# Kernel optimization log

Measured on AMD Instinct MI355X. Metric: run time of the kernel, lower is better.

The kernel has to match this reference:

```python
import jax, jax.numpy as jnp
import numpy as np

NUM_LAYERS = 4
B, L, D = 8, 512, 512
H, F = 8, 2048
HD = D // H
EPS = 1e-5


def _layernorm(x, g, b):
    mu = jnp.mean(x, axis=-1, keepdims=True)
    var = jnp.var(x, axis=-1, keepdims=True)
    return (x - mu) * jax.lax.rsqrt(var + EPS) * g + b


def setup_inputs() -> dict:
    key = jax.random.key(0)
    ks = jax.random.split(key, 14)
    s = 0.02
    return {
        "src": jax.random.normal(ks[0], (B, L, D), dtype=jnp.float32),
        "Wqkv": jax.random.normal(ks[1], (NUM_LAYERS, 3 * D, D), dtype=jnp.float32) * s,
        "bqkv": jnp.zeros((NUM_LAYERS, 3 * D), dtype=jnp.float32),
        "Wo": jax.random.normal(ks[2], (NUM_LAYERS, D, D), dtype=jnp.float32) * s,
        "bo": jnp.zeros((NUM_LAYERS, D), dtype=jnp.float32),
        "W1": jax.random.normal(ks[3], (NUM_LAYERS, F, D), dtype=jnp.float32) * s,
        "b1": jnp.zeros((NUM_LAYERS, F), dtype=jnp.float32),
        "W2": jax.random.normal(ks[4], (NUM_LAYERS, D, F), dtype=jnp.float32) * s,
        "b2": jnp.zeros((NUM_LAYERS, D), dtype=jnp.float32),
        "g1": jnp.ones((NUM_LAYERS, D), dtype=jnp.float32),
        "be1": jnp.zeros((NUM_LAYERS, D), dtype=jnp.float32),
        "g2": jnp.ones((NUM_LAYERS, D), dtype=jnp.float32),
        "be2": jnp.zeros((NUM_LAYERS, D), dtype=jnp.float32),
    }


def reference(src, Wqkv, bqkv, Wo, bo, W1, b1, W2, b2, g1, be1, g2, be2):
    x = src
    attns = []
    scale = 1.0 / np.sqrt(HD).astype(np.float32)
    for i in range(NUM_LAYERS):
        # --- self attention (need_weights=True, average_attn_weights=False) ---
        qkv = x @ Wqkv[i].T + bqkv[i]                      # [B,L,3D]
        q, k, v = jnp.split(qkv, 3, axis=-1)
        q = q.reshape(B, L, H, HD).transpose(0, 2, 1, 3)   # [B,H,L,hd]
        k = k.reshape(B, L, H, HD).transpose(0, 2, 1, 3)
        v = v.reshape(B, L, H, HD).transpose(0, 2, 1, 3)
        scores = jnp.einsum("bhld,bhsd->bhls", q * scale, k)
        attn = jax.nn.softmax(scores, axis=-1)             # [B,H,L,S]
        attns.append(attn)
        ctx = jnp.einsum("bhls,bhsd->bhld", attn, v)
        ctx = ctx.transpose(0, 2, 1, 3).reshape(B, L, D)
        attn_out = ctx @ Wo[i].T + bo[i]
        # --- post-norm residual + FFN ---
        x = _layernorm(x + attn_out, g1[i], be1[i])
        ff = jax.nn.relu(x @ W1[i].T + b1[i]) @ W2[i].T + b2[i]
        x = _layernorm(x + ff, g2[i], be2[i])
    return x, jnp.stack(attns)  # ([B,L,D], [num_layers,B,H,L,S])
```

## Files before the change

kernel.cpp:

```cpp
#include <hip/hip_runtime.h>
#include <hip/hip_bf16.h>

#define B_ 8
#define L_ 512
#define D_ 512
#define H_ 8
#define F_ 2048
#define NL_ 4
#define BL 4096
#define EPS_ 1e-5f

typedef __bf16 bf16_t;
typedef bf16_t bf16x8 __attribute__((ext_vector_type(8)));
typedef float f32x4 __attribute__((ext_vector_type(4)));
typedef unsigned short u16x4 __attribute__((ext_vector_type(4)));

__device__ __forceinline__ unsigned short f2b_rn(float f) {
  unsigned u = __builtin_bit_cast(unsigned, f);
  u = (u + 0x7fffu + ((u >> 16) & 1u)) >> 16;
  return (unsigned short)u;
}

__device__ __forceinline__ void gload_lds16(const unsigned short* g, unsigned short* l) {
  __builtin_amdgcn_global_load_lds(
      (const __attribute__((address_space(1))) void*)g,
      (__attribute__((address_space(3))) void*)l, 16, 0, 0);
}

template<int BM, int BN, int MT, int NT>
__global__ __launch_bounds__(256)
void gemm_bt(const unsigned short* __restrict__ A, int lda, long sAo, long sAi,
             const unsigned short* __restrict__ Bm, int ldb, long sBo, long sBi,
             float* __restrict__ Cf, unsigned short* __restrict__ Cb, int ldc,
             long sCo, long sCi,
             const float* __restrict__ bias, int K, float scale, int relu, int zi)
{
  static_assert(BM == MT * 32 && BN == NT * 32, "waves are 2x2");
  __shared__ unsigned short As[BM * 32];
  __shared__ unsigned short Bs[BN * 32];
  const int tid  = threadIdx.x;
  const int lane = tid & 63;
  const int wave = tid >> 6;
  const int wm = (wave >> 1) * (MT * 16);
  const int wn = (wave & 1) * (NT * 16);
  const int m0 = blockIdx.x * BM;
  const int n0 = blockIdx.y * BN;
  const int z  = blockIdx.z;
  const long offA = (long)(z / zi) * sAo + (long)(z % zi) * sAi;
  const long offB = (long)(z / zi) * sBo + (long)(z % zi) * sBi;
  const long offC = (long)(z / zi) * sCo + (long)(z % zi) * sCi;

  f32x4 acc[MT][NT] = {};

  for (int k0 = 0; k0 < K; k0 += 32) {
    __syncthreads();
#pragma unroll
    for (int j = 0; j < BM / 64; ++j) {
      int c = tid + j * 256;
      int r = c >> 2, cc = (c & 3) * 8;
      gload_lds16(A + offA + (long)(m0 + r) * lda + (k0 + cc), &As[c * 8]);
    }
#pragma unroll
    for (int j = 0; j < BN / 64; ++j) {
      int c = tid + j * 256;
      int r = c >> 2, cc = (c & 3) * 8;
      gload_lds16(Bm + offB + (long)(n0 + r) * ldb + (k0 + cc), &Bs[c * 8]);
    }
    __syncthreads();
    bf16x8 af[MT], bfr[NT];
#pragma unroll
    for (int mt = 0; mt < MT; ++mt)
      af[mt] = *(const bf16x8*)(&As[(wm + mt * 16 + (lane & 15)) * 32 + (lane >> 4) * 8]);
#pragma unroll
    for (int nt = 0; nt < NT; ++nt)
      bfr[nt] = *(const bf16x8*)(&Bs[(wn + nt * 16 + (lane & 15)) * 32 + (lane >> 4) * 8]);
#pragma unroll
    for (int mt = 0; mt < MT; ++mt)
#pragma unroll
      for (int nt = 0; nt < NT; ++nt)
        acc[mt][nt] = __builtin_amdgcn_mfma_f32_16x16x32_bf16(af[mt], bfr[nt], acc[mt][nt], 0, 0, 0);
  }

#pragma unroll
  for (int nt = 0; nt < NT; ++nt) {
    const int col = n0 + wn + nt * 16 + (lane & 15);
    const float bb = bias ? bias[col] : 0.f;
#pragma unroll
    for (int mt = 0; mt < MT; ++mt) {
#pragma unroll
      for (int r = 0; r < 4; ++r) {
        const int row = m0 + wm + mt * 16 + (lane >> 4) * 4 + r;
        float v = acc[mt][nt][r] * scale + bb;
        if (relu) v = fmaxf(v, 0.f);
        const long o = offC + (long)row * ldc + col;
        if (Cf) Cf[o] = v;
        if (Cb) Cb[o] = f2b_rn(v);
      }
    }
  }
}

__global__ __launch_bounds__(256)
void attn_fused(const unsigned short* __restrict__ qkv,
                float* __restrict__ attnf,
                unsigned short* __restrict__ ctxb) {
  __shared__ __align__(16) unsigned short Qs[64 * 64];
  __shared__ __align__(16) unsigned short KP[512 * 64];
  __shared__ __align__(16) unsigned short VT[64 * 512];
  const int tid = threadIdx.x, lane = tid & 63, wave = tid >> 6;
  const int lo4 = lane & 15, hi4 = lane >> 4;
  const int q0 = blockIdx.x * 64;
  const int z = blockIdx.y, b = z >> 3, h = z & 7;
  const unsigned short* qbase = qkv + (long)b * 512 * 1536 + h * 64;
  const unsigned short* kbase = qbase + 512;
  const unsigned short* vbase = qbase + 1024;

  bf16x8 vreg[16];
#pragma unroll
  for (int j = 0; j < 16; ++j) {
    const int d8 = j >> 1;
    const int s = (j & 1) * 256 + tid;
    vreg[j] = *(const bf16x8*)(vbase + (long)s * 1536 + d8 * 8);
  }

#pragma unroll
  for (int j = 0; j < 2; ++j) {
    int c = tid + j * 256;
    int r = c >> 3, cc = (c & 7) * 8;
    gload_lds16(qbase + (long)(q0 + r) * 1536 + cc, &Qs[c * 8]);
  }
#pragma unroll
  for (int j = 0; j < 16; ++j) {
    int c = tid + j * 256;
    int r = c >> 3, ch = (c & 7) ^ (r & 7);
    gload_lds16(kbase + (long)r * 1536 + ch * 8, &KP[c * 8]);
  }
  __syncthreads();

  const bf16x8 af0 = *(const bf16x8*)&Qs[(wave * 16 + lo4) * 64 + hi4 * 8];
  const bf16x8 af1 = *(const bf16x8*)&Qs[(wave * 16 + lo4) * 64 + 32 + hi4 * 8];

  f32x4 acc[32];
#pragma unroll
  for (int st = 0; st < 32; ++st) {
    const int n = st * 16 + lo4;
    const int sw = n & 7;
    f32x4 a = {};
    const bf16x8 b0 = *(const bf16x8*)&KP[n * 64 + ((hi4 ^ sw) * 8)];
    const bf16x8 b1 = *(const bf16x8*)&KP[n * 64 + (((hi4 + 4) ^ sw) * 8)];
    a = __builtin_amdgcn_mfma_f32_16x16x32_bf16(af0, b0, a, 0, 0, 0);
    a = __builtin_amdgcn_mfma_f32_16x16x32_bf16(af1, b1, a, 0, 0, 0);
    acc[st] = a;
  }

  float mx[4] = {-1e30f, -1e30f, -1e30f, -1e30f};
#pragma unroll
  for (int st = 0; st < 32; ++st)
#pragma unroll
    for (int r = 0; r < 4; ++r) {
      acc[st][r] *= 0.125f;
      mx[r] = fmaxf(mx[r], acc[st][r]);
    }
#pragma unroll
  for (int msk = 1; msk < 16; msk <<= 1)
#pragma unroll
    for (int r = 0; r < 4; ++r) mx[r] = fmaxf(mx[r], __shfl_xor(mx[r], msk));
  float sm[4] = {0.f, 0.f, 0.f, 0.f};
#pragma unroll
  for (int st = 0; st < 32; ++st)
#pragma unroll
    for (int r = 0; r < 4; ++r) {
      const float e = __expf(acc[st][r] - mx[r]);
      acc[st][r] = e;
      sm[r] += e;
    }
#pragma unroll
  for (int msk = 1; msk < 16; msk <<= 1)
#pragma unroll
    for (int r = 0; r < 4; ++r) sm[r] += __shfl_xor(sm[r], msk);
  float inv[4];
#pragma unroll
  for (int r = 0; r < 4; ++r) inv[r] = 1.f / sm[r];

  __syncthreads();

#pragma unroll
  for (int j = 0; j < 16; ++j) {
    const int d8 = j >> 1;
    const int s = (j & 1) * 256 + tid;
#pragma unroll
    for (int jj = 0; jj < 8; ++jj) {
      const int d = d8 * 8 + jj;
      VT[(d * 512 + s) ^ ((d & 7) << 3)] = ((const unsigned short*)&vreg[j])[jj];
    }
  }

  const long obase = (long)z * 262144 + (long)(q0 + wave * 16 + hi4 * 4) * 512 + lo4;
  const int qloc = wave * 16 + hi4 * 4;
#pragma unroll
  for (int st = 0; st < 32; ++st)
#pragma unroll
    for (int r = 0; r < 4; ++r) {
      const float v = acc[st][r] * inv[r];
      attnf[obase + (long)r * 512 + st * 16] = v;
      const int q = qloc + r;
      const int s = st * 16 + lo4;
      KP[(q * 512 + s) ^ ((q & 7) << 3)] = f2b_rn(v);
    }
  __syncthreads();

  const int wm = (wave >> 1) * 32, wn = (wave & 1) * 32;
  f32x4 acc2[2][2] = {};
#pragma unroll
  for (int k0 = 0; k0 < 512; k0 += 32) {
    bf16x8 pa[2], vb[2];
#pragma unroll
    for (int mt = 0; mt < 2; ++mt) {
      const int m = wm + mt * 16 + lo4;
      pa[mt] = *(const bf16x8*)&KP[(m * 512 + k0 + hi4 * 8) ^ ((m & 7) << 3)];
    }
#pragma unroll
    for (int nt = 0; nt < 2; ++nt) {
      const int n = wn + nt * 16 + lo4;
      vb[nt] = *(const bf16x8*)&VT[(n * 512 + k0 + hi4 * 8) ^ ((n & 7) << 3)];
    }
#pragma unroll
    for (int mt = 0; mt < 2; ++mt)
#pragma unroll
      for (int nt = 0; nt < 2; ++nt)
        acc2[mt][nt] = __builtin_amdgcn_mfma_f32_16x16x32_bf16(pa[mt], vb[nt], acc2[mt][nt], 0, 0, 0);
  }

#pragma unroll
  for (int nt = 0; nt < 2; ++nt) {
    const int d = wn + nt * 16 + lo4;
#pragma unroll
    for (int mt = 0; mt < 2; ++mt)
#pragma unroll
      for (int r = 0; r < 4; ++r) {
        const int q = q0 + wm + mt * 16 + hi4 * 4 + r;
        ctxb[((long)(b * 512 + q)) * 512 + h * 64 + d] = f2b_rn(acc2[mt][nt][r]);
      }
  }
}

__global__ __launch_bounds__(128)
void resid_ln(const float* __restrict__ a, const float* __restrict__ b,
              const float* __restrict__ g, const float* __restrict__ be,
              float* __restrict__ outf, unsigned short* __restrict__ outb) {
  const long row = blockIdx.x;
  const int t = threadIdx.x;
  const int wave = t >> 6, lane = t & 63;
  const f32x4 va = *(const f32x4*)&a[row * 512 + t * 4];
  const f32x4 vb = *(const f32x4*)&b[row * 512 + t * 4];
  f32x4 v;
  float s = 0.f, s2 = 0.f;
#pragma unroll
  for (int i = 0; i < 4; ++i) { v[i] = va[i] + vb[i]; s += v[i]; s2 += v[i] * v[i]; }
  for (int o = 32; o > 0; o >>= 1) { s += __shfl_down(s, o); s2 += __shfl_down(s2, o); }
  __shared__ float red[4];
  if (lane == 0) { red[wave] = s; red[2 + wave] = s2; }
  __syncthreads();
  s = red[0] + red[1];
  s2 = red[2] + red[3];
  const float mu  = s * (1.f / 512.f);
  const float var = s2 * (1.f / 512.f) - mu * mu;
  const float ri = rsqrtf(var + EPS_);
  const f32x4 vg = *(const f32x4*)&g[t * 4];
  const f32x4 ve = *(const f32x4*)&be[t * 4];
  f32x4 y;
  u16x4 yb;
#pragma unroll
  for (int i = 0; i < 4; ++i) { y[i] = (v[i] - mu) * ri * vg[i] + ve[i]; yb[i] = f2b_rn(y[i]); }
  *(f32x4*)&outf[row * 512 + t * 4] = y;
  *(u16x4*)&outb[row * 512 + t * 4] = yb;
}

__global__ void f2b_arr(const float* __restrict__ in, unsigned short* __restrict__ out, long n4) {
  long i = (long)blockIdx.x * 256 + threadIdx.x;
  const long stride = (long)gridDim.x * 256;
  for (; i < n4; i += stride) {
    const f32x4 v = *(const f32x4*)&in[i * 4];
    u16x4 o;
#pragma unroll
    for (int k = 0; k < 4; ++k) o[k] = f2b_rn(v[k]);
    *(u16x4*)&out[i * 4] = o;
  }
}

__global__ void copy_conv(const float* __restrict__ in, float* __restrict__ outf,
                          unsigned short* __restrict__ outb, long n4) {
  long i = (long)blockIdx.x * 256 + threadIdx.x;
  const long stride = (long)gridDim.x * 256;
  for (; i < n4; i += stride) {
    const f32x4 v = *(const f32x4*)&in[i * 4];
    u16x4 o;
#pragma unroll
    for (int k = 0; k < 4; ++k) o[k] = f2b_rn(v[k]);
    *(f32x4*)&outf[i * 4] = v;
    *(u16x4*)&outb[i * 4] = o;
  }
}

extern "C" void kernel_launch(void* const* d_in, const int* in_sizes, int n_in,
                              void* d_out, int out_size, void* d_ws, size_t ws_size,
                              hipStream_t stream) {
  const float* src  = (const float*)d_in[0];
  const float* Wqkv = (const float*)d_in[1];
  const float* bqkv = (const float*)d_in[2];
  const float* Wo   = (const float*)d_in[3];
  const float* bo   = (const float*)d_in[4];
  const float* W1   = (const float*)d_in[5];
  const float* b1   = (const float*)d_in[6];
  const float* W2   = (const float*)d_in[7];
  const float* b2   = (const float*)d_in[8];
  const float* g1   = (const float*)d_in[9];
  const float* be1  = (const float*)d_in[10];
  const float* g2   = (const float*)d_in[11];
  const float* be2  = (const float*)d_in[12];

  char* p = (char*)d_ws;
  auto take = [&](size_t bytes) { void* r = (void*)p; p += (bytes + 255) & ~(size_t)255; return r; };
  float* x        = (float*)take((size_t)BL * 512 * 4);
  float* x1       = (float*)take((size_t)BL * 512 * 4);
  float* attn_out = (float*)take((size_t)BL * 512 * 4);
  float* ff2      = (float*)take((size_t)BL * 512 * 4);
  unsigned short* xbf    = (unsigned short*)take((size_t)BL * 512 * 2);
  unsigned short* qkvbf  = (unsigned short*)take((size_t)BL * 1536 * 2);
  unsigned short* ctxbf  = (unsigned short*)take((size_t)BL * 512 * 2);
  unsigned short* ff1bf  = (unsigned short*)take((size_t)BL * 2048 * 2);
  unsigned short* Wqkvb  = (unsigned short*)take((size_t)4 * 1536 * 512 * 2);
  unsigned short* Wob    = (unsigned short*)take((size_t)4 * 512 * 512 * 2);
  unsigned short* W1b    = (unsigned short*)take((size_t)4 * 2048 * 512 * 2);
  unsigned short* W2b    = (unsigned short*)take((size_t)4 * 512 * 2048 * 2);

  f2b_arr<<<1024, 256, 0, stream>>>(Wqkv, Wqkvb, 4L * 1536 * 512 / 4);
  f2b_arr<<<512,  256, 0, stream>>>(Wo,   Wob,   4L * 512 * 512 / 4);
  f2b_arr<<<1024, 256, 0, stream>>>(W1,   W1b,   4L * 2048 * 512 / 4);
  f2b_arr<<<1024, 256, 0, stream>>>(W2,   W2b,   4L * 512 * 2048 / 4);
  copy_conv<<<1024, 256, 0, stream>>>(src, x, xbf, (long)BL * 512 / 4);

  float* out_x    = (float*)d_out;
  float* out_attn = out_x + (size_t)BL * 512;

  for (int i = 0; i < NL_; ++i) {
    gemm_bt<128, 128, 4, 4><<<dim3(BL / 128, 1536 / 128, 1), 256, 0, stream>>>(
        xbf, 512, 0, 0, Wqkvb + (size_t)i * 1536 * 512, 512, 0, 0,
        nullptr, qkvbf, 1536, 0, 0, bqkv + (size_t)i * 1536, 512, 1.f, 0, 1);

    float* attnL = out_attn + (size_t)i * 64 * 512 * 512;
    attn_fused<<<dim3(8, 64), 256, 0, stream>>>(qkvbf, attnL, ctxbf);

    gemm_bt<128, 64, 4, 2><<<dim3(32, 8, 1), 256, 0, stream>>>(
        ctxbf, 512, 0, 0, Wob + (size_t)i * 512 * 512, 512, 0, 0,
        attn_out, nullptr, 512, 0, 0, bo + (size_t)i * 512, 512, 1.f, 0, 1);

    resid_ln<<<BL, 128, 0, stream>>>(x, attn_out, g1 + (size_t)i * 512, be1 + (size_t)i * 512, x1, xbf);

    gemm_bt<128, 128, 4, 4><<<dim3(32, 16, 1), 256, 0, stream>>>(
        xbf, 512, 0, 0, W1b + (size_t)i * 2048 * 512, 512, 0, 0,
        nullptr, ff1bf, 2048, 0, 0, b1 + (size_t)i * 2048, 512, 1.f, 1, 1);

    gemm_bt<128, 64, 4, 2><<<dim3(32, 8, 1), 256, 0, stream>>>(
        ff1bf, 2048, 0, 0, W2b + (size_t)i * 512 * 2048, 2048, 0, 0,
        ff2, nullptr, 512, 0, 0, b2 + (size_t)i * 512, 2048, 1.f, 0, 1);

    resid_ln<<<BL, 128, 0, stream>>>(x1, ff2, g2 + (size_t)i * 512, be2 + (size_t)i * 512,
                                     (i == 3) ? out_x : x, xbf);
  }
}
```

Baseline: 881.5 us.

## Transpose attention MFMA operands, remap blocks per XCD, vectorize attn stores

```diff
diff --git a/kernel.cpp b/kernel.cpp
--- a/kernel.cpp
+++ b/kernel.cpp
@@ -43,8 +43,17 @@
   const int wave = tid >> 6;
   const int wm = (wave >> 1) * (MT * 16);
   const int wn = (wave & 1) * (NT * 16);
-  const int m0 = blockIdx.x * BM;
-  const int n0 = blockIdx.y * BN;
+  int bx = blockIdx.x, by = blockIdx.y;
+  if (gridDim.z == 1 && (gridDim.x & 7) == 0) {
+    const int gx = gridDim.x, cx = gx >> 3;
+    const int lid = by * gx + bx;
+    const int xcd = lid & 7;
+    const int t = lid >> 3;
+    bx = xcd * cx + (t % cx);
+    by = t / cx;
+  }
+  const int m0 = bx * BM;
+  const int n0 = by * BN;
   const int z  = blockIdx.z;
   const long offA = (long)(z / zi) * sAo + (long)(z % zi) * sAi;
   const long offB = (long)(z / zi) * sBo + (long)(z % zi) * sBi;
@@ -109,8 +118,16 @@
   __shared__ __align__(16) unsigned short VT[64 * 512];
   const int tid = threadIdx.x, lane = tid & 63, wave = tid >> 6;
   const int lo4 = lane & 15, hi4 = lane >> 4;
-  const int q0 = blockIdx.x * 64;
-  const int z = blockIdx.y, b = z >> 3, h = z & 7;
+  int bxr = blockIdx.x, byr = blockIdx.y;
+  {
+    const int lid = byr * 8 + bxr;
+    const int xcd = lid & 7;
+    const int t = lid >> 3;
+    byr = xcd * 8 + (t & 7);
+    bxr = t >> 3;
+  }
+  const int q0 = bxr * 64;
+  const int z = byr, b = z >> 3, h = z & 7;
   const unsigned short* qbase = qkv + (long)b * 512 * 1536 + h * 64;
   const unsigned short* kbase = qbase + 512;
   const unsigned short* vbase = qbase + 1024;
@@ -137,50 +154,44 @@
   }
   __syncthreads();
 
-  const bf16x8 af0 = *(const bf16x8*)&Qs[(wave * 16 + lo4) * 64 + hi4 * 8];
-  const bf16x8 af1 = *(const bf16x8*)&Qs[(wave * 16 + lo4) * 64 + 32 + hi4 * 8];
+  const bf16x8 qf0 = *(const bf16x8*)&Qs[(wave * 16 + lo4) * 64 + hi4 * 8];
+  const bf16x8 qf1 = *(const bf16x8*)&Qs[(wave * 16 + lo4) * 64 + 32 + hi4 * 8];
 
   f32x4 acc[32];
 #pragma unroll
   for (int st = 0; st < 32; ++st) {
     const int n = st * 16 + lo4;
-    const int sw = n & 7;
+    const int sw = lo4 & 7;
     f32x4 a = {};
-    const bf16x8 b0 = *(const bf16x8*)&KP[n * 64 + ((hi4 ^ sw) * 8)];
-    const bf16x8 b1 = *(const bf16x8*)&KP[n * 64 + (((hi4 + 4) ^ sw) * 8)];
-    a = __builtin_amdgcn_mfma_f32_16x16x32_bf16(af0, b0, a, 0, 0, 0);
-    a = __builtin_amdgcn_mfma_f32_16x16x32_bf16(af1, b1, a, 0, 0, 0);
+    const bf16x8 k0f = *(const bf16x8*)&KP[n * 64 + ((hi4 ^ sw) * 8)];
+    const bf16x8 k1f = *(const bf16x8*)&KP[n * 64 + (((hi4 + 4) ^ sw) * 8)];
+    a = __builtin_amdgcn_mfma_f32_16x16x32_bf16(k0f, qf0, a, 0, 0, 0);
+    a = __builtin_amdgcn_mfma_f32_16x16x32_bf16(k1f, qf1, a, 0, 0, 0);
     acc[st] = a;
   }
 
-  float mx[4] = {-1e30f, -1e30f, -1e30f, -1e30f};
+  float mx = -1e30f;
 #pragma unroll
   for (int st = 0; st < 32; ++st)
 #pragma unroll
     for (int r = 0; r < 4; ++r) {
       acc[st][r] *= 0.125f;
-      mx[r] = fmaxf(mx[r], acc[st][r]);
-    }
-#pragma unroll
-  for (int msk = 1; msk < 16; msk <<= 1)
-#pragma unroll
-    for (int r = 0; r < 4; ++r) mx[r] = fmaxf(mx[r], __shfl_xor(mx[r], msk));
-  float sm[4] = {0.f, 0.f, 0.f, 0.f};
+      mx = fmaxf(mx, acc[st][r]);
+    }
+  mx = fmaxf(mx, __shfl_xor(mx, 16));
+  mx = fmaxf(mx, __shfl_xor(mx, 32));
+  float sm = 0.f;
 #pragma unroll
   for (int st = 0; st < 32; ++st)
 #pragma unroll
     for (int r = 0; r < 4; ++r) {
-      const float e = __expf(acc[st][r] - mx[r]);
+      const float e = __expf(acc[st][r] - mx);
       acc[st][r] = e;
-      sm[r] += e;
-    }
-#pragma unroll
-  for (int msk = 1; msk < 16; msk <<= 1)
-#pragma unroll
-    for (int r = 0; r < 4; ++r) sm[r] += __shfl_xor(sm[r], msk);
-  float inv[4];
-#pragma unroll
-  for (int r = 0; r < 4; ++r) inv[r] = 1.f / sm[r];
+      sm += e;
+    }
+  sm += __shfl_xor(sm, 16);
+  sm += __shfl_xor(sm, 32);
+  const float inv = 1.f / sm;
 
   __syncthreads();
 
@@ -195,52 +206,55 @@
     }
   }
 
-  const long obase = (long)z * 262144 + (long)(q0 + wave * 16 + hi4 * 4) * 512 + lo4;
-  const int qloc = wave * 16 + hi4 * 4;
-#pragma unroll
-  for (int st = 0; st < 32; ++st)
+  const int q = wave * 16 + lo4;
+  float* aout = attnf + (long)z * 262144 + (long)(q0 + q) * 512;
+#pragma unroll
+  for (int st = 0; st < 32; ++st) {
+    f32x4 pv;
+    u16x4 pb;
 #pragma unroll
     for (int r = 0; r < 4; ++r) {
-      const float v = acc[st][r] * inv[r];
-      attnf[obase + (long)r * 512 + st * 16] = v;
-      const int q = qloc + r;
-      const int s = st * 16 + lo4;
-      KP[(q * 512 + s) ^ ((q & 7) << 3)] = f2b_rn(v);
-    }
+      pv[r] = acc[st][r] * inv;
+      pb[r] = f2b_rn(pv[r]);
+    }
+    __builtin_nontemporal_store(pv, (f32x4*)(aout + st * 16 + hi4 * 4));
+    *(u16x4*)&KP[(q * 512 + st * 16 + hi4 * 4) ^ ((q & 7) << 3)] = pb;
+  }
   __syncthreads();
 
-  const int wm = (wave >> 1) * 32, wn = (wave & 1) * 32;
+  const int wq = (wave >> 1) * 32, wd = (wave & 1) * 32;
   f32x4 acc2[2][2] = {};
 #pragma unroll
   for (int k0 = 0; k0 < 512; k0 += 32) {
-    bf16x8 pa[2], vb[2];
+    bf16x8 vf[2], pf[2];
 #pragma unroll
     for (int mt = 0; mt < 2; ++mt) {
-      const int m = wm + mt * 16 + lo4;
-      pa[mt] = *(const bf16x8*)&KP[(m * 512 + k0 + hi4 * 8) ^ ((m & 7) << 3)];
+      const int d = wd + mt * 16 + lo4;
+      vf[mt] = *(const bf16x8*)&VT[(d * 512 + k0 + hi4 * 8) ^ ((d & 7) << 3)];
     }
 #pragma unroll
     for (int nt = 0; nt < 2; ++nt) {
-      const int n = wn + nt * 16 + lo4;
-      vb[nt] = *(const bf16x8*)&VT[(n * 512 + k0 + hi4 * 8) ^ ((n & 7) << 3)];
+      const int m = wq + nt * 16 + lo4;
+      pf[nt] = *(const bf16x8*)&KP[(m * 512 + k0 + hi4 * 8) ^ ((m & 7) << 3)];
     }
 #pragma unroll
     for (int mt = 0; mt < 2; ++mt)
 #pragma unroll
       for (int nt = 0; nt < 2; ++nt)
-        acc2[mt][nt] = __builtin_amdgcn_mfma_f32_16x16x32_bf16(pa[mt], vb[nt], acc2[mt][nt], 0, 0, 0);
+        acc2[mt][nt] = __builtin_amdgcn_mfma_f32_16x16x32_bf16(vf[mt], pf[nt], acc2[mt][nt], 0, 0, 0);
   }
 
 #pragma unroll
   for (int nt = 0; nt < 2; ++nt) {
-    const int d = wn + nt * 16 + lo4;
-#pragma unroll
-    for (int mt = 0; mt < 2; ++mt)
-#pragma unroll
-      for (int r = 0; r < 4; ++r) {
-        const int q = q0 + wm + mt * 16 + hi4 * 4 + r;
-        ctxb[((long)(b * 512 + q)) * 512 + h * 64 + d] = f2b_rn(acc2[mt][nt][r]);
-      }
+    const int qq = q0 + wq + nt * 16 + lo4;
+    unsigned short* cb = ctxb + ((long)(b * 512 + qq)) * 512 + h * 64;
+#pragma unroll
+    for (int mt = 0; mt < 2; ++mt) {
+      u16x4 o;
+#pragma unroll
+      for (int r = 0; r < 4; ++r) o[r] = f2b_rn(acc2[mt][nt][r]);
+      *(u16x4*)&cb[wd + mt * 16 + hi4 * 4] = o;
+    }
   }
 }
 
@@ -344,7 +358,7 @@
   float* out_attn = out_x + (size_t)BL * 512;
 
   for (int i = 0; i < NL_; ++i) {
-    gemm_bt<128, 128, 4, 4><<<dim3(BL / 128, 1536 / 128, 1), 256, 0, stream>>>(
+    gemm_bt<64, 128, 2, 4><<<dim3(BL / 64, 1536 / 128, 1), 256, 0, stream>>>(
         xbf, 512, 0, 0, Wqkvb + (size_t)i * 1536 * 512, 512, 0, 0,
         nullptr, qkvbf, 1536, 0, 0, bqkv + (size_t)i * 1536, 512, 1.f, 0, 1);
 
```

Measured after the change: 842.9 us. -4.4%, faster.
